# Performance work log

Measured on AMD Instinct MI355X. Metric: run time of the kernel, lower is better.

The kernel has to match this reference:

```python
import jax, jax.numpy as jnp
import numpy as np

B, S, D, H = 2, 2048, 4096, 32
HD = D // H  # 128

def _rope(t, cos, sin):
    # t: [B,S,H,HD]; cos,sin: [S,HD//2]; interleaved complex pairs on last dim
    b, s, h, d = t.shape
    tr = t.reshape(b, s, h, d // 2, 2)
    x0, x1 = tr[..., 0], tr[..., 1]
    c = cos[None, :, None, :]
    sn = sin[None, :, None, :]
    o0 = x0 * c - x1 * sn
    o1 = x0 * sn + x1 * c
    return jnp.stack([o0, o1], axis=-1).reshape(b, s, h, d)

def setup_inputs() -> dict:
    key = jax.random.key(0)
    ks = jax.random.split(key, 6)
    x = jax.random.normal(ks[0], (B, S, D), dtype=jnp.float32)
    theta = 10000.0 ** (-jnp.arange(0, HD, 2, dtype=jnp.float32) / HD)  # [HD//2]
    ang = jnp.arange(S, dtype=jnp.float32)[:, None] * theta[None, :]    # [S, HD//2]
    freqs_cos, freqs_sin = jnp.cos(ang), jnp.sin(ang)
    # additive causal mask [S,S]
    mask = jnp.where(jnp.triu(jnp.ones((S, S), dtype=bool), k=1), -1e9, 0.0).astype(jnp.float32)
    std = 1.0 / np.sqrt(D)
    wq = jax.random.normal(ks[1], (D, D), dtype=jnp.float32) * std
    wk = jax.random.normal(ks[2], (D, D), dtype=jnp.float32) * std
    wv = jax.random.normal(ks[3], (D, D), dtype=jnp.float32) * std
    wo = jax.random.normal(ks[4], (D, D), dtype=jnp.float32) * std
    return {"x": x, "freqs_cos": freqs_cos, "freqs_sin": freqs_sin, "mask": mask,
            "wq": wq, "wk": wk, "wv": wv, "wo": wo, "start_pos": 0}

def reference(x, freqs_cos, freqs_sin, mask, wq, wk, wv, wo, start_pos):
    b, s, d = x.shape
    # Linear layers: torch nn.Linear stores weight [out,in] -> x @ W.T
    xq = (x @ wq.T).reshape(b, s, H, HD)
    xk = (x @ wk.T).reshape(b, s, H, HD)
    xv = (x @ wv.T).reshape(b, s, H, HD)
    xq = _rope(xq, freqs_cos, freqs_sin)
    xk = _rope(xk, freqs_cos, freqs_sin)
    # prefill (start_pos=0): cache slice [:, :s] == xk, xv
    scale = 1.0 / jnp.sqrt(jnp.float32(HD))
    scores = jnp.einsum("bqhd,bkhd->bhqk", xq, xk) * scale + mask[None, None, :, :]
    probs = jax.nn.softmax(scores, axis=-1)
    out = jnp.einsum("bhqk,bkhd->bqhd", probs, xv).reshape(b, s, d)
    return out @ wo.T
```

## Files before the change

### kernel.cpp

```cpp
#include <hip/hip_runtime.h>
#include <hip/hip_bf16.h>
#include <math.h>

typedef unsigned short u16;
typedef __bf16 bf16x8 __attribute__((ext_vector_type(8)));
typedef float f32x4 __attribute__((ext_vector_type(4)));

#define B_  2
#define S_  2048
#define D_  4096
#define H_  32
#define HD_ 128

__device__ __forceinline__ unsigned rne_bf16(float x) {
  unsigned u = __float_as_uint(x);
  return (u + 0x7fffu + ((u >> 16) & 1u)) >> 16;
}

__device__ __forceinline__ void async16(void* lds, const void* g) {
  __builtin_amdgcn_global_load_lds(
      (__attribute__((address_space(1))) void*)(g),
      (__attribute__((address_space(3))) void*)(lds), 16, 0, 0);
}

__global__ __launch_bounds__(256) void convert_bf16(
    const float* __restrict__ src, u16* __restrict__ dst, int n8) {
  int i = blockIdx.x * 256 + threadIdx.x;
  if (i >= n8) return;
  const float4* s = (const float4*)src + (size_t)i * 2;
  float4 a = s[0], b = s[1];
  uint4 o;
  o.x = rne_bf16(a.x) | (rne_bf16(a.y) << 16);
  o.y = rne_bf16(a.z) | (rne_bf16(a.w) << 16);
  o.z = rne_bf16(b.x) | (rne_bf16(b.y) << 16);
  o.w = rne_bf16(b.z) | (rne_bf16(b.w) << 16);
  ((uint4*)dst)[i] = o;
}

template <int MODE>
__global__ __launch_bounds__(256) void gemm_bt(
    const u16* __restrict__ A, const u16* __restrict__ Bw,
    u16* __restrict__ outB, float* __restrict__ outF,
    const float* __restrict__ fc, const float* __restrict__ fs) {
  __shared__ u16 As[128 * 32];
  __shared__ u16 Bs[128 * 32];
  const int tid  = threadIdx.x;
  const int lane = tid & 63;
  const int wave = tid >> 6;
  const int lm   = lane & 15, quad = lane >> 4;
  const int m0 = blockIdx.x * 128, n0 = blockIdx.y * 128;
  const int mr = (wave >> 1) * 64, nc = (wave & 1) * 64;
  const int K = 4096;

  const int c0 = tid, c1 = tid + 256;
  const int r0 = c0 >> 2, kc0 = ((c0 & 3) ^ ((c0 >> 4) & 3)) * 8;
  const int r1 = c1 >> 2, kc1 = ((c1 & 3) ^ ((c1 >> 4) & 3)) * 8;
  const u16* Ag0 = A + (size_t)(m0 + r0) * K + kc0;
  const u16* Ag1 = A + (size_t)(m0 + r1) * K + kc1;
  const u16* Bg0 = Bw + (size_t)(n0 + r0) * K + kc0;
  const u16* Bg1 = Bw + (size_t)(n0 + r1) * K + kc1;

  const int koff = (quad ^ ((lm >> 2) & 3)) * 8;

  f32x4 acc[4][4] = {};

  for (int kb = 0; kb < K; kb += 32) {
    async16(&As[c0 * 8], Ag0 + kb);
    async16(&As[c1 * 8], Ag1 + kb);
    async16(&Bs[c0 * 8], Bg0 + kb);
    async16(&Bs[c1 * 8], Bg1 + kb);
    __syncthreads();
    bf16x8 af[4], bfr[4];
#pragma unroll
    for (int i = 0; i < 4; ++i) af[i] = *(const bf16x8*)&As[(mr + i * 16 + lm) * 32 + koff];
#pragma unroll
    for (int j = 0; j < 4; ++j) bfr[j] = *(const bf16x8*)&Bs[(nc + j * 16 + lm) * 32 + koff];
#pragma unroll
    for (int i = 0; i < 4; ++i)
#pragma unroll
      for (int j = 0; j < 4; ++j)
        acc[i][j] = __builtin_amdgcn_mfma_f32_16x16x32_bf16(af[i], bfr[j], acc[i][j], 0, 0, 0);
    __syncthreads();
  }

  if (MODE == 1) {
#pragma unroll
    for (int i = 0; i < 4; ++i) {
      const int mbase = m0 + mr + i * 16 + quad * 4;
#pragma unroll
      for (int j = 0; j < 4; ++j) {
        const int n = n0 + nc + j * 16 + lm;
        const int h = n >> 7, d = n & 127, ir = d >> 1;
#pragma unroll
        for (int r = 0; r < 4; ++r) {
          const int m = mbase + r;
          const int s = m & (S_ - 1);
          const int bb = m >> 11;
          float v = acc[i][j][r];
          float p = __shfl_xor(v, 1);
          float cv = fc[s * (HD_ / 2) + ir];
          float sv = fs[s * (HD_ / 2) + ir];
          float o = ((lane & 1) == 0) ? (v * cv - p * sv) : (p * sv + v * cv);
          float po = __shfl_xor(o, 1);
          if ((lane & 1) == 0) {
            unsigned pkt = rne_bf16(o) | (rne_bf16(po) << 16);
            size_t idx = (((size_t)(bb * H_ + h) * S_ + s) * HD_ + d) >> 1;
            ((unsigned*)outB)[idx] = pkt;
          }
        }
      }
    }
  } else if (MODE == 3) {
#pragma unroll
    for (int i = 0; i < 4; ++i) {
      const int mbase = m0 + mr + i * 16 + quad * 4;
      const int s0 = mbase & (S_ - 1);
      const int bb = mbase >> 11;
#pragma unroll
      for (int j = 0; j < 4; ++j) {
        const int n = n0 + nc + j * 16 + lm;
        const int h = n >> 7, d = n & 127;
        uint2 pkt;
        pkt.x = rne_bf16(acc[i][j][0]) | (rne_bf16(acc[i][j][1]) << 16);
        pkt.y = rne_bf16(acc[i][j][2]) | (rne_bf16(acc[i][j][3]) << 16);
        size_t idx = ((size_t)(bb * H_ + h) * HD_ + d) * S_ + s0;
        *(uint2*)&outB[idx] = pkt;
      }
    }
  } else {
#pragma unroll
    for (int i = 0; i < 4; ++i) {
      const int mbase = m0 + mr + i * 16 + quad * 4;
#pragma unroll
      for (int j = 0; j < 4; ++j) {
        const int n = n0 + nc + j * 16 + lm;
#pragma unroll
        for (int r = 0; r < 4; ++r) outF[(size_t)(mbase + r) * D_ + n] = acc[i][j][r];
      }
    }
  }
}

__global__ __launch_bounds__(256, 2) void flash_attn(
    const u16* __restrict__ Qb, const u16* __restrict__ Kb,
    const u16* __restrict__ Vtb, u16* __restrict__ attn) {
  __shared__ __align__(16) u16 lds[32768];

  const int tid = threadIdx.x;
  const int lane = tid & 63, w = tid >> 6;
  const int lm = lane & 15, quad = lane >> 4;
  const int qb = 15 - blockIdx.x;
  const int bh = blockIdx.y;
  const int bb = bh >> 5, h = bh & 31;

  const u16* Qg = Qb + ((size_t)bh * S_ + qb * 128 + w * 32) * HD_;
  const u16* Kg = Kb + (size_t)bh * S_ * HD_;
  const u16* Vg = Vtb + (size_t)bh * HD_ * S_;

  const u16* kp[4];
  const u16* vp[4];
#pragma unroll
  for (int it = 0; it < 4; ++it) {
    int c = tid + 256 * it;
    int kr = c >> 4, kc = (c & 15) ^ (kr & 15);
    kp[it] = Kg + (size_t)kr * HD_ + kc * 8;
    int vr = c >> 3, vc = (c & 7) ^ (vr & 7);
    vp[it] = Vg + (size_t)vr * S_ + vc * 8;
  }

  bf16x8 qf[2][4];
#pragma unroll
  for (int qt = 0; qt < 2; ++qt)
#pragma unroll
    for (int dk = 0; dk < 4; ++dk)
      qf[qt][dk] = *(const bf16x8*)(Qg + (size_t)(qt * 16 + lm) * HD_ + dk * 32 + quad * 8);

  f32x4 accO[8][2] = {};
  float m_run[2] = {-1e30f, -1e30f}, l_run[2] = {0.f, 0.f};
  const float scale = 0.08838834764831845f;
  const int nkt = 2 * qb + 2;
  const int qg0 = qb * 128 + w * 32;
  const int wq_max = qg0 + 31;

#pragma unroll
  for (int it = 0; it < 4; ++it) {
    async16(&lds[(tid + 256 * it) * 8], kp[it]);
    async16(&lds[8192 + (tid + 256 * it) * 8], vp[it]);
  }

  for (int kt = 0; kt < nkt; ++kt) {
    const int k0 = kt * 64;
    const int cur = (kt & 1) * 16384;
    __syncthreads();
    if (kt + 1 < nkt) {
      const int nxt = cur ^ 16384;
      const size_t koK = (size_t)(kt + 1) * 64 * HD_;
      const size_t koV = (size_t)(kt + 1) * 64;
#pragma unroll
      for (int it = 0; it < 4; ++it) {
        async16(&lds[nxt + (tid + 256 * it) * 8], kp[it] + koK);
        async16(&lds[nxt + 8192 + (tid + 256 * it) * 8], vp[it] + koV);
      }
    }
    if (k0 <= wq_max) {
      const u16* Ks = lds + cur;
      const u16* Vts = lds + cur + 8192;
      f32x4 sacc[2][4] = {};
#pragma unroll
      for (int dk = 0; dk < 4; ++dk) {
        bf16x8 kf[4];
#pragma unroll
        for (int t = 0; t < 4; ++t) {
          int row = (t >> 1) * 32 + ((lm >> 2) * 8) + ((t & 1) * 4) + (lm & 3);
          int ch = (dk * 4 + quad) ^ (row & 15);
          kf[t] = *(const bf16x8*)&Ks[(row * 16 + ch) * 8];
        }
#pragma unroll
        for (int t = 0; t < 4; ++t)
#pragma unroll
          for (int qt = 0; qt < 2; ++qt)
            sacc[qt][t] = __builtin_amdgcn_mfma_f32_16x16x32_bf16(kf[t], qf[qt][dk], sacc[qt][t], 0, 0, 0);
      }
      if (k0 + 63 > qg0) {
#pragma unroll
        for (int qt = 0; qt < 2; ++qt) {
          int q = qg0 + qt * 16 + lm;
#pragma unroll
          for (int t = 0; t < 4; ++t) {
            int kb = k0 + (t >> 1) * 32 + quad * 8 + (t & 1) * 4;
#pragma unroll
            for (int r = 0; r < 4; ++r)
              if (kb + r > q) sacc[qt][t][r] = -1e30f;
          }
        }
      }
      bf16x8 pf[2][2];
      float alpha[2];
#pragma unroll
      for (int qt = 0; qt < 2; ++qt) {
        float tmax = sacc[qt][0][0];
#pragma unroll
        for (int t = 0; t < 4; ++t)
#pragma unroll
          for (int r = 0; r < 4; ++r) tmax = fmaxf(tmax, sacc[qt][t][r]);
        tmax = fmaxf(tmax, __shfl_xor(tmax, 16));
        tmax = fmaxf(tmax, __shfl_xor(tmax, 32));
        float mnew = fmaxf(m_run[qt], tmax);
        alpha[qt] = __expf((m_run[qt] - mnew) * scale);
        m_run[qt] = mnew;
        float ms = mnew * scale;
        float rs = 0.f;
#pragma unroll
        for (int t = 0; t < 4; ++t)
#pragma unroll
          for (int r = 0; r < 4; ++r) {
            float p = __expf(fmaf(sacc[qt][t][r], scale, -ms));
            sacc[qt][t][r] = p;
            rs += p;
          }
        rs += __shfl_xor(rs, 16);
        rs += __shfl_xor(rs, 32);
        l_run[qt] = l_run[qt] * alpha[qt] + rs;
#pragma unroll
        for (int kc = 0; kc < 2; ++kc)
#pragma unroll
          for (int j = 0; j < 4; ++j) {
            pf[kc][qt][j]     = (__bf16)sacc[qt][2 * kc][j];
            pf[kc][qt][j + 4] = (__bf16)sacc[qt][2 * kc + 1][j];
          }
      }
#pragma unroll
      for (int dt = 0; dt < 8; ++dt)
#pragma unroll
        for (int qt = 0; qt < 2; ++qt)
#pragma unroll
          for (int r = 0; r < 4; ++r) accO[dt][qt][r] *= alpha[qt];
#pragma unroll
      for (int kc = 0; kc < 2; ++kc)
#pragma unroll
        for (int dt = 0; dt < 8; ++dt) {
          int row = dt * 16 + lm;
          int ch = (kc * 4 + quad) ^ (row & 7);
          bf16x8 vf = *(const bf16x8*)&Vts[(row * 8 + ch) * 8];
#pragma unroll
          for (int qt = 0; qt < 2; ++qt)
            accO[dt][qt] = __builtin_amdgcn_mfma_f32_16x16x32_bf16(vf, pf[kc][qt], accO[dt][qt], 0, 0, 0);
        }
    }
  }

  __syncthreads();
  u16* Et = lds;
  float inv[2] = {1.f / l_run[0], 1.f / l_run[1]};
#pragma unroll
  for (int dt = 0; dt < 8; ++dt)
#pragma unroll
    for (int qt = 0; qt < 2; ++qt) {
      const int rowq = w * 32 + qt * 16 + lm;
#pragma unroll
      for (int rp = 0; rp < 2; ++rp) {
        float a0 = accO[dt][qt][rp * 2] * inv[qt];
        float a1 = accO[dt][qt][rp * 2 + 1] * inv[qt];
        unsigned pkt = rne_bf16(a0) | (rne_bf16(a1) << 16);
        *(unsigned*)&Et[rowq * 136 + dt * 16 + quad * 4 + rp * 2] = pkt;
      }
    }
  const int rloc = w * 32 + (lane >> 1);
  const int half = lane & 1;
  const size_t gbase = (size_t)(bb * S_ + qb * 128 + rloc) * D_ + h * 128 + half * 64;
#pragma unroll
  for (int k = 0; k < 8; ++k) {
    uint4 vv = *(const uint4*)&Et[rloc * 136 + half * 64 + k * 8];
    *(uint4*)&attn[gbase + k * 8] = vv;
  }
}

extern "C" void kernel_launch(void* const* d_in, const int* in_sizes, int n_in,
                              void* d_out, int out_size, void* d_ws, size_t ws_size,
                              hipStream_t stream) {
  const float* x  = (const float*)d_in[0];
  const float* fc = (const float*)d_in[1];
  const float* fs = (const float*)d_in[2];
  const float* wq = (const float*)d_in[4];
  const float* wk = (const float*)d_in[5];
  const float* wv = (const float*)d_in[6];
  const float* wo = (const float*)d_in[7];
  float* out = (float*)d_out;

  char* ws = (char*)d_ws;
  const size_t SZ = (size_t)B_ * S_ * D_ * 2;
  u16* xb  = (u16*)(ws);
  u16* wqb = (u16*)(ws + SZ);
  u16* wkb = (u16*)(ws + 2 * SZ);
  u16* wvb = (u16*)(ws + 3 * SZ);
  u16* Qb  = (u16*)(ws + 4 * SZ);
  u16* Kb  = (u16*)(ws + 5 * SZ);
  u16* Vtb = (u16*)(ws + 6 * SZ);
  u16* attn = xb;
  u16* wob  = wqb;

  dim3 blk(256);
  const int n8 = (B_ * S_ * D_) / 8;
  convert_bf16<<<n8 / 256, blk, 0, stream>>>(x, xb, n8);
  convert_bf16<<<n8 / 256, blk, 0, stream>>>(wq, wqb, n8);
  convert_bf16<<<n8 / 256, blk, 0, stream>>>(wk, wkb, n8);
  convert_bf16<<<n8 / 256, blk, 0, stream>>>(wv, wvb, n8);

  dim3 g1(32, 32);
  gemm_bt<1><<<g1, blk, 0, stream>>>(xb, wqb, Qb, nullptr, fc, fs);
  gemm_bt<1><<<g1, blk, 0, stream>>>(xb, wkb, Kb, nullptr, fc, fs);
  gemm_bt<3><<<g1, blk, 0, stream>>>(xb, wvb, Vtb, nullptr, nullptr, nullptr);

  dim3 g2(16, 64);
  flash_attn<<<g2, blk, 0, stream>>>(Qb, Kb, Vtb, attn);

  convert_bf16<<<n8 / 256, blk, 0, stream>>>(wo, wob, n8);
  gemm_bt<4><<<g1, blk, 0, stream>>>(attn, wob, nullptr, out, nullptr, nullptr);
}
```

Measured before the change: 1.269 ms.

## Rewrite GEMM as 256x256 tile, 8-wave double-buffered pipelined kernel

Replaces the simple 128x128, single-buffered GEMM with a 256x256 tile per 512-thread block. It uses a 64-wide K step, a double-buffered swizzled LDS layout (128 KB), and an interleaved schedule of async global-to-LDS loads, LDS reads and MFMA quadrants with explicit barriers, waitcnts and setprio. It also adds a block-index swizzle for L2 locality. The goal is to hide load latency behind MFMA and raise arithmetic intensity in the four projection GEMMs. The cost is much higher register and LDS pressure, and a complex hand schedule that is fragile to get right.

```diff
diff --git a/kernel.cpp b/kernel.cpp
--- a/kernel.cpp
+++ b/kernel.cpp
@@ -17,10 +17,10 @@
   return (u + 0x7fffu + ((u >> 16) & 1u)) >> 16;
 }
 
-__device__ __forceinline__ void async16(void* lds, const void* g) {
+__device__ __forceinline__ void async16(void* lds_p, const void* g) {
   __builtin_amdgcn_global_load_lds(
       (__attribute__((address_space(1))) void*)(g),
-      (__attribute__((address_space(3))) void*)(lds), 16, 0, 0);
+      (__attribute__((address_space(3))) void*)(lds_p), 16, 0, 0);
 }
 
 __global__ __launch_bounds__(256) void convert_bf16(
@@ -37,60 +37,177 @@
   ((uint4*)dst)[i] = o;
 }
 
+
+#define WGBAR() asm volatile("s_barrier" ::: "memory")
+#define LGKM0() do { asm volatile("s_waitcnt lgkmcnt(0)" ::: "memory"); \
+                     __builtin_amdgcn_sched_barrier(0); } while (0)
+#define VMW(N)  asm volatile("s_waitcnt vmcnt(" #N ")" ::: "memory")
+
+#define STAGE_A(P, HH, T) do { \
+  async16(&lds[(P) * 32768 + (HH) * 8192 + c0 * 8], Ag[HH][0] + (size_t)(T) * 64); \
+  async16(&lds[(P) * 32768 + (HH) * 8192 + c1 * 8], Ag[HH][1] + (size_t)(T) * 64); \
+} while (0)
+#define STAGE_B(P, HH, T) do { \
+  async16(&lds[(P) * 32768 + 16384 + (HH) * 8192 + c0 * 8], Bg[HH][0] + (size_t)(T) * 64); \
+  async16(&lds[(P) * 32768 + 16384 + (HH) * 8192 + c1 * 8], Bg[HH][1] + (size_t)(T) * 64); \
+} while (0)
+
+#define READ_A(dst, P, MH) do { \
+  _Pragma("unroll") for (int i_ = 0; i_ < 4; ++i_) \
+  _Pragma("unroll") for (int kk_ = 0; kk_ < 2; ++kk_) \
+    dst[i_][kk_] = *(const bf16x8*)&lds[(P) * 32768 + ((MH) * 4 + i_) * 1024 + aoff[kk_]]; \
+} while (0)
+#define READ_B(dst, P, NH) do { \
+  _Pragma("unroll") for (int j_ = 0; j_ < 2; ++j_) \
+  _Pragma("unroll") for (int kk_ = 0; kk_ < 2; ++kk_) \
+    dst[j_][kk_] = *(const bf16x8*)&lds[(P) * 32768 + ((NH) * 2 + j_) * 1024 + boff[kk_]]; \
+} while (0)
+
+#define MFMA_Q(AF, BF, IB, JB) do { \
+  __builtin_amdgcn_s_setprio(1); \
+  _Pragma("unroll") for (int kk_ = 0; kk_ < 2; ++kk_) \
+  _Pragma("unroll") for (int i_ = 0; i_ < 4; ++i_) \
+  _Pragma("unroll") for (int j_ = 0; j_ < 2; ++j_) \
+    acc[(IB) + i_][(JB) + j_] = __builtin_amdgcn_mfma_f32_16x16x32_bf16( \
+        AF[i_][kk_], BF[j_][kk_], acc[(IB) + i_][(JB) + j_], 0, 0, 0); \
+  __builtin_amdgcn_s_setprio(0); \
+} while (0)
+
 template <int MODE>
-__global__ __launch_bounds__(256) void gemm_bt(
+__global__ __launch_bounds__(512, 2) void gemm_bt(
     const u16* __restrict__ A, const u16* __restrict__ Bw,
     u16* __restrict__ outB, float* __restrict__ outF,
     const float* __restrict__ fc, const float* __restrict__ fs) {
-  __shared__ u16 As[128 * 32];
-  __shared__ u16 Bs[128 * 32];
-  const int tid  = threadIdx.x;
+  __shared__ __align__(16) u16 lds[65536];
+
+  const int tid = threadIdx.x;
   const int lane = tid & 63;
-  const int wave = tid >> 6;
-  const int lm   = lane & 15, quad = lane >> 4;
-  const int m0 = blockIdx.x * 128, n0 = blockIdx.y * 128;
-  const int mr = (wave >> 1) * 64, nc = (wave & 1) * 64;
+  const int w = tid >> 6;
+  const int lm = lane & 15, quad = lane >> 4;
+  const int wr = w >> 2, wc = w & 3;
   const int K = 4096;
-
-  const int c0 = tid, c1 = tid + 256;
-  const int r0 = c0 >> 2, kc0 = ((c0 & 3) ^ ((c0 >> 4) & 3)) * 8;
-  const int r1 = c1 >> 2, kc1 = ((c1 & 3) ^ ((c1 >> 4) & 3)) * 8;
-  const u16* Ag0 = A + (size_t)(m0 + r0) * K + kc0;
-  const u16* Ag1 = A + (size_t)(m0 + r1) * K + kc1;
-  const u16* Bg0 = Bw + (size_t)(n0 + r0) * K + kc0;
-  const u16* Bg1 = Bw + (size_t)(n0 + r1) * K + kc1;
-
-  const int koff = (quad ^ ((lm >> 2) & 3)) * 8;
-
-  f32x4 acc[4][4] = {};
-
-  for (int kb = 0; kb < K; kb += 32) {
-    async16(&As[c0 * 8], Ag0 + kb);
-    async16(&As[c1 * 8], Ag1 + kb);
-    async16(&Bs[c0 * 8], Bg0 + kb);
-    async16(&Bs[c1 * 8], Bg1 + kb);
-    __syncthreads();
-    bf16x8 af[4], bfr[4];
-#pragma unroll
-    for (int i = 0; i < 4; ++i) af[i] = *(const bf16x8*)&As[(mr + i * 16 + lm) * 32 + koff];
-#pragma unroll
-    for (int j = 0; j < 4; ++j) bfr[j] = *(const bf16x8*)&Bs[(nc + j * 16 + lm) * 32 + koff];
-#pragma unroll
-    for (int i = 0; i < 4; ++i)
-#pragma unroll
-      for (int j = 0; j < 4; ++j)
-        acc[i][j] = __builtin_amdgcn_mfma_f32_16x16x32_bf16(af[i], bfr[j], acc[i][j], 0, 0, 0);
-    __syncthreads();
-  }
+  const int NKT = K / 64;
+
+  const int bid = blockIdx.x;
+  const int swz = (bid & 7) * 32 + (bid >> 3);
+  const int m0 = (swz >> 4) * 256, n0 = (swz & 15) * 256;
+
+  const int c0 = tid, c1 = tid + 512;
+  const int rl0 = c0 >> 3, s0 = ((c0 & 7) ^ (rl0 & 7)) * 8;
+  const int rl1 = c1 >> 3, s1 = ((c1 & 7) ^ (rl1 & 7)) * 8;
+  const u16* Ag[2][2];
+  const u16* Bg[2][2];
+#pragma unroll
+  for (int hh = 0; hh < 2; ++hh) {
+    Ag[hh][0] = A + (size_t)(m0 + hh * 128 + rl0) * K + s0;
+    Ag[hh][1] = A + (size_t)(m0 + hh * 128 + rl1) * K + s1;
+    Bg[hh][0] = Bw + (size_t)(n0 + hh * 128 + rl0) * K + s0;
+    Bg[hh][1] = Bw + (size_t)(n0 + hh * 128 + rl1) * K + s1;
+  }
+
+  int aoff[2], boff[2];
+#pragma unroll
+  for (int kk = 0; kk < 2; ++kk) {
+    const int sw = ((kk * 4 + quad) ^ (lm & 7)) * 8;
+    aoff[kk] = (wr * 128 + lm) * 64 + sw;
+    boff[kk] = 16384 + (wc * 64 + lm) * 64 + sw;
+  }
+
+  bf16x8 aA[4][2], aB[4][2], b0r[2][2], b1r[2][2];
+  f32x4 acc[8][4] = {};
+
+  STAGE_A(0, 0, 0); STAGE_A(0, 1, 0); STAGE_B(0, 0, 0); STAGE_B(0, 1, 0);
+  STAGE_B(1, 0, 1); STAGE_A(1, 0, 1); STAGE_A(1, 1, 1);
+  VMW(6);
+  WGBAR();
+  READ_A(aA, 0, 0);
+  READ_B(b0r, 0, 0);
+
+  for (int kt = 0; kt < NKT - 2; kt += 2) {
+    READ_B(b1r, 0, 1);
+    STAGE_B(1, 1, kt + 1);
+    WGBAR(); LGKM0();
+    MFMA_Q(aA, b0r, 0, 0);
+    WGBAR();
+    READ_A(aB, 0, 1);
+    STAGE_B(0, 0, kt + 2);
+    WGBAR(); LGKM0();
+    MFMA_Q(aA, b1r, 0, 2);
+    VMW(4);
+    WGBAR();
+    READ_A(aA, 1, 0);
+    STAGE_A(0, 0, kt + 2);
+    WGBAR(); LGKM0();
+    MFMA_Q(aB, b1r, 4, 2);
+    VMW(4);
+    WGBAR();
+    READ_B(b1r, 1, 0);
+    STAGE_A(0, 1, kt + 2);
+    WGBAR(); LGKM0();
+    MFMA_Q(aB, b0r, 4, 0);
+    WGBAR();
+    READ_B(b0r, 1, 1);
+    STAGE_B(0, 1, kt + 2);
+    WGBAR(); LGKM0();
+    MFMA_Q(aA, b1r, 0, 0);
+    WGBAR();
+    READ_A(aB, 1, 1);
+    STAGE_B(1, 0, kt + 3);
+    WGBAR(); LGKM0();
+    MFMA_Q(aA, b0r, 0, 2);
+    VMW(4);
+    WGBAR();
+    READ_A(aA, 0, 0);
+    STAGE_A(1, 0, kt + 3);
+    WGBAR(); LGKM0();
+    MFMA_Q(aB, b0r, 4, 2);
+    VMW(4);
+    WGBAR();
+    READ_B(b0r, 0, 0);
+    STAGE_A(1, 1, kt + 3);
+    WGBAR(); LGKM0();
+    MFMA_Q(aB, b1r, 4, 0);
+    WGBAR();
+  }
+
+  READ_B(b1r, 0, 1);
+  STAGE_B(1, 1, NKT - 1);
+  WGBAR(); LGKM0();
+  MFMA_Q(aA, b0r, 0, 0);
+  WGBAR();
+  READ_A(aB, 0, 1);
+  WGBAR(); LGKM0();
+  MFMA_Q(aA, b1r, 0, 2);
+  VMW(2);
+  WGBAR();
+  READ_A(aA, 1, 0);
+  WGBAR(); LGKM0();
+  MFMA_Q(aB, b1r, 4, 2);
+  VMW(0);
+  WGBAR();
+  READ_B(b1r, 1, 0);
+  WGBAR(); LGKM0();
+  MFMA_Q(aB, b0r, 4, 0);
+  WGBAR();
+  READ_B(b0r, 1, 1);
+  WGBAR(); LGKM0();
+  MFMA_Q(aA, b1r, 0, 0);
+  WGBAR();
+  READ_A(aB, 1, 1);
+  WGBAR(); LGKM0();
+  MFMA_Q(aA, b0r, 0, 2);
+  WGBAR();
+  MFMA_Q(aB, b0r, 4, 2);
+  MFMA_Q(aB, b1r, 4, 0);
 
   if (MODE == 1) {
 #pragma unroll
-    for (int i = 0; i < 4; ++i) {
-      const int mbase = m0 + mr + i * 16 + quad * 4;
+    for (int i = 0; i < 8; ++i) {
+      const int mbase = m0 + wr * 128 + i * 16 + quad * 4;
 #pragma unroll
       for (int j = 0; j < 4; ++j) {
-        const int n = n0 + nc + j * 16 + lm;
-        const int h = n >> 7, d = n & 127, ir = d >> 1;
+        const int n = n0 + wc * 64 + j * 16 + lm;
+        const int hh = n >> 7, d = n & 127, ir = d >> 1;
 #pragma unroll
         for (int r = 0; r < 4; ++r) {
           const int m = mbase + r;
@@ -104,7 +221,7 @@
           float po = __shfl_xor(o, 1);
           if ((lane & 1) == 0) {
             unsigned pkt = rne_bf16(o) | (rne_bf16(po) << 16);
-            size_t idx = (((size_t)(bb * H_ + h) * S_ + s) * HD_ + d) >> 1;
+            size_t idx = (((size_t)(bb * H_ + hh) * S_ + s) * HD_ + d) >> 1;
             ((unsigned*)outB)[idx] = pkt;
           }
         }
@@ -112,28 +229,28 @@
     }
   } else if (MODE == 3) {
 #pragma unroll
-    for (int i = 0; i < 4; ++i) {
-      const int mbase = m0 + mr + i * 16 + quad * 4;
-      const int s0 = mbase & (S_ - 1);
+    for (int i = 0; i < 8; ++i) {
+      const int mbase = m0 + wr * 128 + i * 16 + quad * 4;
+      const int sB = mbase & (S_ - 1);
       const int bb = mbase >> 11;
 #pragma unroll
       for (int j = 0; j < 4; ++j) {
-        const int n = n0 + nc + j * 16 + lm;
-        const int h = n >> 7, d = n & 127;
+        const int n = n0 + wc * 64 + j * 16 + lm;
+        const int hh = n >> 7, d = n & 127;
         uint2 pkt;
         pkt.x = rne_bf16(acc[i][j][0]) | (rne_bf16(acc[i][j][1]) << 16);
         pkt.y = rne_bf16(acc[i][j][2]) | (rne_bf16(acc[i][j][3]) << 16);
-        size_t idx = ((size_t)(bb * H_ + h) * HD_ + d) * S_ + s0;
+        size_t idx = ((size_t)(bb * H_ + hh) * HD_ + d) * S_ + sB;
         *(uint2*)&outB[idx] = pkt;
       }
     }
   } else {
 #pragma unroll
-    for (int i = 0; i < 4; ++i) {
-      const int mbase = m0 + mr + i * 16 + quad * 4;
+    for (int i = 0; i < 8; ++i) {
+      const int mbase = m0 + wr * 128 + i * 16 + quad * 4;
 #pragma unroll
       for (int j = 0; j < 4; ++j) {
-        const int n = n0 + nc + j * 16 + lm;
+        const int n = n0 + wc * 64 + j * 16 + lm;
 #pragma unroll
         for (int r = 0; r < 4; ++r) outF[(size_t)(mbase + r) * D_ + n] = acc[i][j][r];
       }
@@ -346,14 +463,15 @@
   convert_bf16<<<n8 / 256, blk, 0, stream>>>(wk, wkb, n8);
   convert_bf16<<<n8 / 256, blk, 0, stream>>>(wv, wvb, n8);
 
-  dim3 g1(32, 32);
-  gemm_bt<1><<<g1, blk, 0, stream>>>(xb, wqb, Qb, nullptr, fc, fs);
-  gemm_bt<1><<<g1, blk, 0, stream>>>(xb, wkb, Kb, nullptr, fc, fs);
-  gemm_bt<3><<<g1, blk, 0, stream>>>(xb, wvb, Vtb, nullptr, nullptr, nullptr);
+  dim3 blkG(512);
+  dim3 g1(256);
+  gemm_bt<1><<<g1, blkG, 0, stream>>>(xb, wqb, Qb, nullptr, fc, fs);
+  gemm_bt<1><<<g1, blkG, 0, stream>>>(xb, wkb, Kb, nullptr, fc, fs);
+  gemm_bt<3><<<g1, blkG, 0, stream>>>(xb, wvb, Vtb, nullptr, nullptr, nullptr);
 
   dim3 g2(16, 64);
   flash_attn<<<g2, blk, 0, stream>>>(Qb, Kb, Vtb, attn);
 
   convert_bf16<<<n8 / 256, blk, 0, stream>>>(wo, wob, n8);
-  gemm_bt<4><<<g1, blk, 0, stream>>>(attn, wob, nullptr, out, nullptr, nullptr);
-}
+  gemm_bt<4><<<g1, blkG, 0, stream>>>(attn, wob, nullptr, out, nullptr, nullptr);
+}
```

New measurement: 1.632 ms. +28.6%, slower.

## Double-buffer GEMM LDS tiles, remap block order, and change swizzle

Applied to the files above, without the earlier changes.

Turns the GEMM main loop into a double-buffered pipeline that issues the global-to-LDS loads for the next K tile while the current one is computed, so load latency overlaps the MFMA work. It also remaps block indices into grouped tiles for better L2 reuse of the A and B panels, changes the LDS XOR swizzle pattern, and adds an occupancy hint to launch bounds. LDS use doubles per block, which can lower occupancy. The block remap hardcodes a 32-wide grid shape.

```diff
diff --git a/kernel.cpp b/kernel.cpp
--- a/kernel.cpp
+++ b/kernel.cpp
@@ -17,10 +17,10 @@
   return (u + 0x7fffu + ((u >> 16) & 1u)) >> 16;
 }
 
-__device__ __forceinline__ void async16(void* lds, const void* g) {
+__device__ __forceinline__ void async16(void* lds_p, const void* g) {
   __builtin_amdgcn_global_load_lds(
       (__attribute__((address_space(1))) void*)(g),
-      (__attribute__((address_space(3))) void*)(lds), 16, 0, 0);
+      (__attribute__((address_space(3))) void*)(lds_p), 16, 0, 0);
 }
 
 __global__ __launch_bounds__(256) void convert_bf16(
@@ -38,38 +38,53 @@
 }
 
 template <int MODE>
-__global__ __launch_bounds__(256) void gemm_bt(
+__global__ __launch_bounds__(256, 3) void gemm_bt(
     const u16* __restrict__ A, const u16* __restrict__ Bw,
     u16* __restrict__ outB, float* __restrict__ outF,
     const float* __restrict__ fc, const float* __restrict__ fs) {
-  __shared__ u16 As[128 * 32];
-  __shared__ u16 Bs[128 * 32];
+  __shared__ __align__(16) u16 lds[16384];
   const int tid  = threadIdx.x;
   const int lane = tid & 63;
   const int wave = tid >> 6;
   const int lm   = lane & 15, quad = lane >> 4;
-  const int m0 = blockIdx.x * 128, n0 = blockIdx.y * 128;
   const int mr = (wave >> 1) * 64, nc = (wave & 1) * 64;
   const int K = 4096;
-
-  const int c0 = tid, c1 = tid + 256;
-  const int r0 = c0 >> 2, kc0 = ((c0 & 3) ^ ((c0 >> 4) & 3)) * 8;
-  const int r1 = c1 >> 2, kc1 = ((c1 & 3) ^ ((c1 >> 4) & 3)) * 8;
-  const u16* Ag0 = A + (size_t)(m0 + r0) * K + kc0;
-  const u16* Ag1 = A + (size_t)(m0 + r1) * K + kc1;
-  const u16* Bg0 = Bw + (size_t)(n0 + r0) * K + kc0;
-  const u16* Bg1 = Bw + (size_t)(n0 + r1) * K + kc1;
-
-  const int koff = (quad ^ ((lm >> 2) & 3)) * 8;
+  const int NT = K / 32;
+
+  const int bid = blockIdx.y * 32 + blockIdx.x;
+  const int xg = bid & 7, l = bid >> 3;
+  const int m0 = (((xg & 3) * 8) + (l & 7)) * 128;
+  const int n0 = (((xg >> 2) * 16) + (l >> 3)) * 128;
+
+  const int ca = tid, cb = tid + 256;
+  const int ra = ca >> 2, ga = ((ca & 3) ^ ((ca >> 3) & 3)) * 8;
+  const int rb = cb >> 2, gb = ((cb & 3) ^ ((cb >> 3) & 3)) * 8;
+  const u16* Ag0 = A + (size_t)(m0 + ra) * K + ga;
+  const u16* Ag1 = A + (size_t)(m0 + rb) * K + gb;
+  const u16* Bg0 = Bw + (size_t)(n0 + ra) * K + ga;
+  const u16* Bg1 = Bw + (size_t)(n0 + rb) * K + gb;
+
+  const int koff = (quad ^ ((lm >> 1) & 3)) * 8;
 
   f32x4 acc[4][4] = {};
 
-  for (int kb = 0; kb < K; kb += 32) {
-    async16(&As[c0 * 8], Ag0 + kb);
-    async16(&As[c1 * 8], Ag1 + kb);
-    async16(&Bs[c0 * 8], Bg0 + kb);
-    async16(&Bs[c1 * 8], Bg1 + kb);
-    __syncthreads();
+  async16(&lds[ca * 8], Ag0);
+  async16(&lds[cb * 8], Ag1);
+  async16(&lds[4096 + ca * 8], Bg0);
+  async16(&lds[4096 + cb * 8], Bg1);
+  __syncthreads();
+
+  for (int t = 0; t < NT; ++t) {
+    const u16* As = lds + (t & 1) * 8192;
+    const u16* Bs = As + 4096;
+    if (t < NT - 1) {
+      u16* Ld = lds + ((t + 1) & 1) * 8192;
+      const size_t ko = (size_t)(t + 1) * 32;
+      async16(&Ld[ca * 8], Ag0 + ko);
+      async16(&Ld[cb * 8], Ag1 + ko);
+      async16(&Ld[4096 + ca * 8], Bg0 + ko);
+      async16(&Ld[4096 + cb * 8], Bg1 + ko);
+    }
     bf16x8 af[4], bfr[4];
 #pragma unroll
     for (int i = 0; i < 4; ++i) af[i] = *(const bf16x8*)&As[(mr + i * 16 + lm) * 32 + koff];
```

New measurement: 1.126 ms. 1.13x faster.
